# Kernel tuning notes

Hardware: AMD Instinct MI355X
Metric: run time of the kernel (lower is better)

Reference implementation:

```python
import jax, jax.numpy as jnp
import numpy as np
import math

B = 512
EMB = 512
CLASSNUM = 70722
M = 0.4
H = 0.333
S = 64.0
EPS = 1e-3


def setup_inputs() -> dict:
    key = jax.random.key(0)
    k1, k2, k3, k4, k5 = jax.random.split(key, 5)
    embbedings = jax.random.normal(k1, (B, EMB), dtype=jnp.float32)
    # feature norms: positive, realistic range ~[1, 30)
    norms = jax.random.uniform(k2, (B, 1), dtype=jnp.float32) * 29.0 + 1.0
    label = jax.random.randint(k3, (B,), 0, CLASSNUM, dtype=jnp.int64)
    class_sample_num_ = jax.random.uniform(k4, (B,), dtype=jnp.float32) * 9.0 + 1.0
    kernel = jax.random.normal(k5, (EMB, CLASSNUM), dtype=jnp.float32)
    return {
        "embbedings": embbedings,
        "norms": norms,
        "label": label,
        "class_sample_num_": class_sample_num_,
        "kernel": kernel,
    }


def reference(embbedings, norms, label, class_sample_num_, kernel):
    # l2-normalize kernel columns (axis=0)
    kernel_norm = kernel / jnp.linalg.norm(kernel, axis=0, keepdims=True)
    cosine = jnp.matmul(embbedings, kernel_norm)  # [B, C]
    cosine = jnp.clip(cosine, -1.0 + EPS, 1.0 - EPS)

    # detached margin scaler path (torch uses .detach / no_grad)
    safe_norms = jnp.clip(norms, 0.001, 100.0)
    safe_norms = safe_norms / (class_sample_num_[:, None] + 0.001)
    safe_norms = jnp.clip(safe_norms, 0.001, 100.0)
    safe_norms = jax.lax.stop_gradient(safe_norms)

    mean = jnp.mean(safe_norms)
    std = jnp.std(safe_norms, ddof=1)  # torch.std is unbiased
    # t_alpha = 1.0 => batch stats are exactly this batch's mean/std
    batch_mean, batch_std = mean, std

    margin_scaler = (safe_norms - batch_mean) / (batch_std + EPS)
    margin_scaler = jnp.clip(margin_scaler * H, -1.0, 1.0)  # [B, 1]
    ms = margin_scaler[:, 0]  # [B]

    rows = jnp.arange(B)
    lab = label.astype(jnp.int32)

    # angular margin: theta_m = clip(theta + onehot * (-m*ms))
    theta = jnp.arccos(cosine)
    theta = theta.at[rows, lab].add(-M * ms)
    theta_m = jnp.clip(theta, EPS, math.pi - EPS)
    cosine2 = jnp.cos(theta_m)

    # additive margin at the label column: g_add = m + m*ms
    cosine2 = cosine2.at[rows, lab].add(-(M + M * ms))

    return cosine2 * S
```

## Files before the change

kernel.cpp:

```cpp
#include <hip/hip_runtime.h>
#include <math.h>

#define CLASSNUM 70722
#define BATCH 512
#define EMBD 512
#define M_C 0.4f
#define H_C 0.333f
#define S_C 64.0f
#define EPS_C 0.001f
#define PI_F 3.14159265358979f

typedef __bf16 bf16_t;
typedef __bf16 bf16x8 __attribute__((ext_vector_type(8)));
typedef float f32x4 __attribute__((ext_vector_type(4)));

__device__ __forceinline__ float clampf(float x, float lo, float hi) {
    return fminf(fmaxf(x, lo), hi);
}

__global__ __launch_bounds__(256) void prep_lab_kernel(
    const float* __restrict__ emb, const float* __restrict__ norms,
    const float* __restrict__ csn, const int* __restrict__ label,
    const float* __restrict__ kmat, bf16_t* __restrict__ Aws,
    float* __restrict__ labout)
{
    __shared__ float red[256];
    const int tid = threadIdx.x;
    const int bi = blockIdx.x;

    if (bi < 128) {
        const int G = bi * 256 + tid;
        const int kt = G >> 11;
        const int rem = G & 2047;
        const int rg = rem >> 6;
        const int lane = rem & 63;
        const int row = rg * 16 + (lane & 15);
        const int k0 = kt * 32 + (lane >> 4) * 8;
        const float* src = emb + row * EMBD + k0;
        const float4 v0 = *(const float4*)src;
        const float4 v1 = *(const float4*)(src + 4);
        bf16x8 bw;
        bw[0] = (bf16_t)v0.x; bw[1] = (bf16_t)v0.y;
        bw[2] = (bf16_t)v0.z; bw[3] = (bf16_t)v0.w;
        bw[4] = (bf16_t)v1.x; bw[5] = (bf16_t)v1.y;
        bw[6] = (bf16_t)v1.z; bw[7] = (bf16_t)v1.w;
        *(bf16x8*)(Aws + (size_t)G * 8) = bw;
        return;
    }

    const int b = bi - 128;

    float s0, s1;
    {
        float sn = clampf(norms[tid], 0.001f, 100.0f);
        sn = sn / (csn[tid] + 0.001f);
        s0 = clampf(sn, 0.001f, 100.0f);
    }
    {
        float sn = clampf(norms[tid + 256], 0.001f, 100.0f);
        sn = sn / (csn[tid + 256] + 0.001f);
        s1 = clampf(sn, 0.001f, 100.0f);
    }
    red[tid] = s0 + s1;
    __syncthreads();
    for (int off = 128; off > 0; off >>= 1) {
        if (tid < off) red[tid] += red[tid + off];
        __syncthreads();
    }
    const float mean = red[0] * (1.0f / 512.0f);
    __syncthreads();
    const float d0 = s0 - mean, d1 = s1 - mean;
    red[tid] = d0 * d0 + d1 * d1;
    __syncthreads();
    for (int off = 128; off > 0; off >>= 1) {
        if (tid < off) red[tid] += red[tid + off];
        __syncthreads();
    }
    const float stdv = sqrtf(red[0] * (1.0f / 511.0f));
    __syncthreads();

    const int lab = label[b];
    const float* col = kmat + lab;
    const float* e = emb + b * EMBD;
    float dot = 0.0f, ss = 0.0f;
#pragma unroll
    for (int k = tid; k < EMBD; k += 256) {
        const float kv = col[(size_t)k * CLASSNUM];
        const float ev = e[k];
        dot = fmaf(ev, kv, dot);
        ss  = fmaf(kv, kv, ss);
    }
    red[tid] = dot;
    __syncthreads();
    for (int off = 128; off > 0; off >>= 1) {
        if (tid < off) red[tid] += red[tid + off];
        __syncthreads();
    }
    const float dotT = red[0];
    __syncthreads();
    red[tid] = ss;
    __syncthreads();
    for (int off = 128; off > 0; off >>= 1) {
        if (tid < off) red[tid] += red[tid + off];
        __syncthreads();
    }
    if (tid == 0) {
        const float ssT = red[0];
        float c = dotT / sqrtf(ssT);
        c = clampf(c, -1.0f + EPS_C, 1.0f - EPS_C);
        float snb = clampf(norms[b], 0.001f, 100.0f);
        snb = snb / (csn[b] + 0.001f);
        snb = clampf(snb, 0.001f, 100.0f);
        const float msv = clampf((snb - mean) / (stdv + EPS_C) * H_C, -1.0f, 1.0f);
        float th = acosf(c) - M_C * msv;
        th = clampf(th, EPS_C, PI_F - EPS_C);
        labout[b] = (cosf(th) - (M_C + M_C * msv)) * S_C;
    }
}


#define LOADB8(t, dst) do {                                             \
    const size_t ko_ = (size_t)((t) * 32) * CLASSNUM;                   \
    _Pragma("unroll")                                                   \
    for (int j_ = 0; j_ < 8; ++j_)                                      \
        dst[j_] = bp[ko_ + (size_t)j_ * CLASSNUM];                      \
} while (0)

#define LOADA4(t, af) do {                                              \
    const bf16x8* ap_ = (const bf16x8*)Aws                              \
        + (((t) * 32 + mbase + wave * 4) * 64 + lane);                  \
    _Pragma("unroll")                                                   \
    for (int mi_ = 0; mi_ < 4; ++mi_) af[mi_] = ap_[mi_ * 64];          \
} while (0)

#define CVTW8(src, buf) do {                                            \
    bf16x8 w_;                                                          \
    _Pragma("unroll")                                                   \
    for (int j_ = 0; j_ < 8; ++j_) {                                    \
        const float v_ = src[j_];                                       \
        ssq = fmaf(v_, v_, ssq);                                        \
        w_[j_] = (bf16_t)v_;                                            \
    }                                                                   \
    *(bf16x8*)&Blds[buf][c * 40 + kg * 8] = w_;                         \
} while (0)

#define MFMA16(af, buf) do {                                            \
    bf16x8 bfr_[4];                                                     \
    _Pragma("unroll")                                                   \
    for (int ni_ = 0; ni_ < 4; ++ni_)                                   \
        bfr_[ni_] = *(const bf16x8*)                                    \
            &Blds[buf][(ni_ * 16 + r16) * 40 + quad * 8];               \
    __builtin_amdgcn_s_setprio(1);                                      \
    _Pragma("unroll")                                                   \
    for (int mi_ = 0; mi_ < 4; ++mi_)                                   \
        _Pragma("unroll")                                               \
        for (int ni_ = 0; ni_ < 4; ++ni_)                               \
            acc[mi_][ni_] = __builtin_amdgcn_mfma_f32_16x16x32_bf16(    \
                af[mi_], bfr_[ni_], acc[mi_][ni_], 0, 0, 0);            \
    __builtin_amdgcn_s_setprio(0);                                      \
} while (0)

#define BARRIER() do {                                                  \
    asm volatile("s_waitcnt lgkmcnt(0)" ::: "memory");                  \
    __builtin_amdgcn_s_barrier();                                       \
} while (0)

__global__ __launch_bounds__(256, 4) void gemm_kernel(
    const bf16_t* __restrict__ Aws, const float* __restrict__ Kmat,
    const int* __restrict__ label, const float* __restrict__ labout,
    float* __restrict__ out)
{
    __shared__ bf16_t Blds[2][64 * 40];
    __shared__ float red[256];
    __shared__ float invn_s[64];
    __shared__ int   lab_s[256];
    __shared__ float lo_s[256];

    const int tid  = threadIdx.x;
    const int lane = tid & 63;
    const int wave = tid >> 6;
    const int r16  = lane & 15;
    const int quad = lane >> 4;

    const int nwg = 2 * ((CLASSNUM + 63) / 64);
    const int q_ = nwg >> 3, r_ = nwg & 7;
    const int xcd = blockIdx.x & 7, idx = blockIdx.x >> 3;
    const int swz = (xcd < r_) ? (xcd * (q_ + 1) + idx)
                               : (r_ * (q_ + 1) + (xcd - r_) * q_ + idx);
    const int mhalf = swz & 1;
    const int n0    = (swz >> 1) * 64;
    const int mbase = mhalf * 16;

    lab_s[tid] = label[mhalf * 256 + tid];
    lo_s[tid]  = labout[mhalf * 256 + tid];

    const int c  = tid & 63;
    const int kg = tid >> 6;
    int cg = n0 + c;
    if (cg >= CLASSNUM) cg = CLASSNUM - 1;
    const float* bp = Kmat + (size_t)(kg * 8) * CLASSNUM + cg;

    f32x4 acc[4][4];
    const f32x4 zero = {0.0f, 0.0f, 0.0f, 0.0f};
#pragma unroll
    for (int i = 0; i < 4; ++i)
#pragma unroll
        for (int j = 0; j < 4; ++j) acc[i][j] = zero;
    float ssq = 0.0f;

    float bv0[8], bv1[8];

    LOADB8(0, bv0);
    LOADB8(1, bv1);
    CVTW8(bv0, 0);
    BARRIER();

#pragma unroll 1
    for (int p = 0; p < 8; ++p) {
        {
            bf16x8 af[4];
            LOADA4(2 * p, af);
            if (p < 7) LOADB8(2 * p + 2, bv0);
            MFMA16(af, 0);
            CVTW8(bv1, 1);
            BARRIER();
        }
        {
            bf16x8 af[4];
            LOADA4(2 * p + 1, af);
            if (p < 7) LOADB8(2 * p + 3, bv1);
            MFMA16(af, 1);
            if (p < 7) CVTW8(bv0, 0);
            BARRIER();
        }
    }

    red[tid] = ssq;
    __syncthreads();
    if (tid < 64) {
        const float s = red[tid] + red[tid + 64] + red[tid + 128] + red[tid + 192];
        invn_s[tid] = (s > 0.0f) ? (1.0f / sqrtf(s)) : 0.0f;
    }
    __syncthreads();

#pragma unroll
    for (int mi = 0; mi < 4; ++mi) {
#pragma unroll
        for (int rr = 0; rr < 4; ++rr) {
            const int rowl = wave * 64 + mi * 16 + quad * 4 + rr;
            const int labc = lab_s[rowl];
            const float lov = lo_s[rowl];
            float* orow = out + (size_t)(mhalf * 256 + rowl) * CLASSNUM;
#pragma unroll
            for (int ni = 0; ni < 4; ++ni) {
                const int col_loc = ni * 16 + r16;
                const int col = n0 + col_loc;
                if (col < CLASSNUM) {
                    const float cc = clampf(acc[mi][ni][rr] * invn_s[col_loc],
                                            -1.0f + EPS_C, 1.0f - EPS_C);
                    float v = cc * S_C;
                    if (labc == col) v = lov;
                    orow[col] = v;
                }
            }
        }
    }
}

extern "C" void kernel_launch(void* const* d_in, const int* in_sizes, int n_in,
                              void* d_out, int out_size, void* d_ws, size_t ws_size,
                              hipStream_t stream)
{
    const float* emb   = (const float*)d_in[0];
    const float* norms = (const float*)d_in[1];
    const int*   label = (const int*)d_in[2];
    const float* csn   = (const float*)d_in[3];
    const float* kmat  = (const float*)d_in[4];
    float* out = (float*)d_out;

    const size_t A_BYTES = (size_t)BATCH * EMBD * sizeof(bf16_t);
    if (ws_size < A_BYTES + 4096) return;
    bf16_t* Aws   = (bf16_t*)d_ws;
    float* labout = (float*)((char*)d_ws + A_BYTES);

    prep_lab_kernel<<<128 + BATCH, 256, 0, stream>>>(
        emb, norms, csn, label, kmat, Aws, labout);
    const int nblk = 2 * ((CLASSNUM + 63) / 64);
    gemm_kernel<<<nblk, 256, 0, stream>>>(Aws, kmat, label, labout, out);
}
```

Baseline: 333.6 us.

## Deepen GEMM software pipeline with triple-buffered B regs and prefetched A

Restructures the K-loop of the cosine GEMM so that global B loads run three stages ahead in a triple register buffer and A fragments are double-buffered and prefetched one step ahead. The loop is also fully unrolled. The aim is to hide global memory latency behind the MFMAs. This raises register pressure, so the occupancy hint in launch bounds drops from 4 to 3 waves per SIMD, which may reduce latency hiding across waves.

```diff
diff --git a/kernel.cpp b/kernel.cpp
--- a/kernel.cpp
+++ b/kernel.cpp
@@ -165,7 +165,7 @@
     __builtin_amdgcn_s_barrier();                                       \
 } while (0)
 
-__global__ __launch_bounds__(256, 4) void gemm_kernel(
+__global__ __launch_bounds__(256, 3) void gemm_kernel(
     const bf16_t* __restrict__ Aws, const float* __restrict__ Kmat,
     const int* __restrict__ label, const float* __restrict__ labout,
     float* __restrict__ out)
@@ -208,31 +208,24 @@
         for (int j = 0; j < 4; ++j) acc[i][j] = zero;
     float ssq = 0.0f;
 
-    float bv0[8], bv1[8];
-
-    LOADB8(0, bv0);
-    LOADB8(1, bv1);
-    CVTW8(bv0, 0);
+    float  bv[3][8];
+    bf16x8 af[2][4];
+
+    LOADB8(0, bv[0]);
+    LOADB8(1, bv[1]);
+    LOADB8(2, bv[2]);
+    LOADA4(0, af[0]);
+    CVTW8(bv[0], 0);
+    LOADB8(3, bv[0]);
     BARRIER();
 
-#pragma unroll 1
-    for (int p = 0; p < 8; ++p) {
-        {
-            bf16x8 af[4];
-            LOADA4(2 * p, af);
-            if (p < 7) LOADB8(2 * p + 2, bv0);
-            MFMA16(af, 0);
-            CVTW8(bv1, 1);
-            BARRIER();
-        }
-        {
-            bf16x8 af[4];
-            LOADA4(2 * p + 1, af);
-            if (p < 7) LOADB8(2 * p + 3, bv1);
-            MFMA16(af, 1);
-            if (p < 7) CVTW8(bv0, 0);
-            BARRIER();
-        }
+#pragma unroll
+    for (int p = 0; p < 16; ++p) {
+        if (p < 15) LOADA4(p + 1, af[(p + 1) & 1]);
+        MFMA16(af[p & 1], p & 1);
+        if (p < 15) CVTW8(bv[(p + 1) % 3], (p + 1) & 1);
+        if (p < 12) LOADB8(p + 4, bv[(p + 1) % 3]);
+        if (p < 15) BARRIER();
     }
 
     red[tid] = ssq;
```

Result: no change. 331.7 us (-0.6%).
